# Optimization experiments

Hardware: AMD Instinct MI355X
Metric: run time of the kernel (lower is better)

Reference implementation:

```python
import jax, jax.numpy as jnp
import numpy as np

N_NODES = 50000
N_EDGES = 800000
D_IN = 512
D_OUT = 256

def setup_inputs() -> dict:
    key = jax.random.key(0)
    k1, k2, k3, k4, k5 = jax.random.split(key, 5)
    return {
        "inputs": jax.random.normal(k1, (N_NODES, D_IN), dtype=jnp.float32),
        "weights": jax.random.uniform(k2, (D_IN, D_OUT), dtype=jnp.float32, minval=-0.1, maxval=0.1),
        "bias": jnp.zeros((D_OUT,), dtype=jnp.float32),
        "edge_vals": jax.random.uniform(k3, (N_EDGES,), dtype=jnp.float32),
        "edge_row": jax.random.randint(k4, (N_EDGES,), 0, N_NODES),
        "edge_col": jax.random.randint(k5, (N_EDGES,), 0, N_NODES),
    }

def reference(inputs, weights, bias, edge_vals, edge_row, edge_col):
    # dense projection: [N, D_in] @ [D_in, D_out] -> [N, D_out]
    supports = inputs @ weights
    # sparse adjacency spmm in COO form: out[i] = sum_e vals[e] * supports[col[e]] for row[e] == i
    msgs = supports[edge_col] * edge_vals[:, None]  # [E, D_out]
    aggregated = jax.ops.segment_sum(msgs, edge_row, num_segments=inputs.shape[0])
    return aggregated + bias
```

## Files before the change

### kernel.cpp

```cpp
#include <hip/hip_runtime.h>

#define D_IN 512
#define D_OUT 256
#define BM 128
#define BN 128
#define BK 32

typedef short short8 __attribute__((ext_vector_type(8)));
typedef float floatx4 __attribute__((ext_vector_type(4)));

static __device__ __forceinline__ unsigned short f2bf(float f) {
    unsigned u = __float_as_uint(f);
    u += 0x7FFF + ((u >> 16) & 1);
    return (unsigned short)(u >> 16);
}
static __device__ __forceinline__ float bf2f(unsigned short h) {
    return __uint_as_float((unsigned)h << 16);
}

#define CONV_BLOCKS 256
__global__ __launch_bounds__(512) void convert_and_zero(const float* __restrict__ W,
                                                        unsigned short* __restrict__ Wt,
                                                        int* __restrict__ cnt, int M) {
    int b = blockIdx.x;
    if (b < CONV_BLOCKS) {
        int t = b * 512 + threadIdx.x;
        int n = t >> 9;
        int k = t & 511;
        Wt[t] = f2bf(W[(size_t)k * D_OUT + n]);
    } else {
        int i = (b - CONV_BLOCKS) * 512 + threadIdx.x;
        if (i < M) cnt[i] = 0;
    }
}

__global__ __launch_bounds__(256) void hist_rows(const int* __restrict__ rows,
                                                 int* __restrict__ cnt, int E) {
    int e = blockIdx.x * 256 + threadIdx.x;
    if (e < E) atomicAdd(&cnt[rows[e]], 1);
}

#define SCAN_B 4096
__global__ __launch_bounds__(1024) void scan_blocks(const int* __restrict__ cnt,
                                                    int* __restrict__ ptr,
                                                    int* __restrict__ partials, int M) {
    __shared__ int wsum[16];
    const int t = threadIdx.x, lane = t & 63, wave = t >> 6;
    const int base = blockIdx.x * SCAN_B + t * 4;
    int4 v = make_int4(0, 0, 0, 0);
    if (base + 3 < M) v = *(const int4*)(cnt + base);
    else {
        if (base + 0 < M) v.x = cnt[base + 0];
        if (base + 1 < M) v.y = cnt[base + 1];
        if (base + 2 < M) v.z = cnt[base + 2];
        if (base + 3 < M) v.w = cnt[base + 3];
    }
    int s = v.x + v.y + v.z + v.w;
    int incl = s;
#pragma unroll
    for (int off = 1; off < 64; off <<= 1) {
        int x = __shfl_up(incl, off, 64);
        if (lane >= off) incl += x;
    }
    if (lane == 63) wsum[wave] = incl;
    __syncthreads();
    if (t == 0) {
        int run = 0;
#pragma unroll
        for (int w = 0; w < 16; ++w) { int x = wsum[w]; wsum[w] = run; run += x; }
        partials[blockIdx.x] = run;
    }
    __syncthreads();
    int e0 = wsum[wave] + (incl - s);
    int e1 = e0 + v.x, e2 = e1 + v.y, e3 = e2 + v.z;
    if (base + 3 < M) *(int4*)(ptr + base) = make_int4(e0, e1, e2, e3);
    else {
        if (base + 0 < M) ptr[base + 0] = e0;
        if (base + 1 < M) ptr[base + 1] = e1;
        if (base + 2 < M) ptr[base + 2] = e2;
        if (base + 3 < M) ptr[base + 3] = e3;
    }
}

__global__ __launch_bounds__(256) void add_offsets(int* __restrict__ ptr,
                                                   const int* __restrict__ partials,
                                                   int M) {
    int i = blockIdx.x * 256 + threadIdx.x;
    if (i >= M) return;
    int bucket = blockIdx.x >> 4;
    int off = 0;
    for (int j = 0; j < bucket; ++j) off += partials[j];
    ptr[i] += off;
}

__global__ __launch_bounds__(512, 4) void gemm_build(
    const float* __restrict__ A, const unsigned short* __restrict__ Wt,
    unsigned short* __restrict__ S, int M, int nGemm, int nBuild,
    const float* __restrict__ vals, const int* __restrict__ rows,
    const int* __restrict__ cols, int* __restrict__ ptr,
    unsigned long long* __restrict__ edges, int E) {
    __shared__ unsigned short As[4 * BM * 8];
    __shared__ unsigned short Bs[4 * BN * 8];
    const int bid = blockIdx.x;
    const int tid = threadIdx.x;
    const int r3  = bid % 3;
    const int p3  = bid / 3;

    if (r3 == 2) {
        if (p3 >= nBuild) return;
        int e0 = p3 * 2048 + tid;
        int rr[4]; unsigned cc[4], vv[4]; bool ok[4];
#pragma unroll
        for (int i = 0; i < 4; ++i) {
            int e = e0 + i * 512;
            ok[i] = e < E;
            int es = ok[i] ? e : 0;
            rr[i] = rows[es];
            cc[i] = (unsigned)cols[es];
            vv[i] = (unsigned)__float_as_int(vals[es]);
        }
#pragma unroll
        for (int i = 0; i < 4; ++i) {
            if (ok[i]) {
                int pos = atomicAdd(&ptr[rr[i]], 1);
                unsigned long long packed =
                    (unsigned long long)cc[i] | ((unsigned long long)vv[i] << 32);
                __builtin_nontemporal_store(packed, edges + pos);
            }
        }
        return;
    }

    const int gi = p3 * 2 + r3;
    if (gi >= nGemm) return;
    const int lane = tid & 63;
    const int wave = tid >> 6;
    const int l15  = lane & 15;
    const int quad = lane >> 4;
    const int bm   = (gi >> 1) * BM;
    const int bn   = (gi & 1) * BN;
    const int wm   = (wave >> 2) * 64;
    const int wn   = (wave & 3) * 32;

    const int sm = wave * 16 + l15;
    const bool aval = (bm + sm) < M;
    const float* aptr = A + (size_t)(aval ? bm + sm : 0) * D_IN + quad * 8;
    const unsigned short* bptr = Wt + (size_t)(bn + sm) * D_IN + quad * 8;
    const int soff = (quad * BM + sm) * 8;

    float4 aR0 = aval ? *(const float4*)(aptr + 0) : make_float4(0.f, 0.f, 0.f, 0.f);
    float4 aR1 = aval ? *(const float4*)(aptr + 4) : make_float4(0.f, 0.f, 0.f, 0.f);
    short8 bR  = *(const short8*)bptr;

    floatx4 acc[4][2] = {};

    for (int k0 = 0; k0 < D_IN; k0 += BK) {
        short8 a8;
        a8[0] = (short)f2bf(aR0.x); a8[1] = (short)f2bf(aR0.y);
        a8[2] = (short)f2bf(aR0.z); a8[3] = (short)f2bf(aR0.w);
        a8[4] = (short)f2bf(aR1.x); a8[5] = (short)f2bf(aR1.y);
        a8[6] = (short)f2bf(aR1.z); a8[7] = (short)f2bf(aR1.w);
        *(short8*)(As + soff) = a8;
        *(short8*)(Bs + soff) = bR;
        __syncthreads();

        if (k0 + BK < D_IN) {
            aR0 = aval ? *(const float4*)(aptr + k0 + BK + 0) : make_float4(0.f, 0.f, 0.f, 0.f);
            aR1 = aval ? *(const float4*)(aptr + k0 + BK + 4) : make_float4(0.f, 0.f, 0.f, 0.f);
            bR  = *(const short8*)(bptr + k0 + BK);
        }

        short8 af[4], bfr[2];
#pragma unroll
        for (int i = 0; i < 4; ++i)
            af[i] = *(const short8*)(As + (quad * BM + wm + i * 16 + l15) * 8);
#pragma unroll
        for (int j = 0; j < 2; ++j)
            bfr[j] = *(const short8*)(Bs + (quad * BN + wn + j * 16 + l15) * 8);
#pragma unroll
        for (int i = 0; i < 4; ++i)
#pragma unroll
            for (int j = 0; j < 2; ++j)
                acc[i][j] = __builtin_amdgcn_mfma_f32_16x16x32_bf16(
                    af[i], bfr[j], acc[i][j], 0, 0, 0);
        __syncthreads();
    }

#pragma unroll
    for (int i = 0; i < 4; ++i) {
#pragma unroll
        for (int r = 0; r < 4; ++r) {
            int gm = bm + wm + i * 16 + quad * 4 + r;
            if (gm < M) {
#pragma unroll
                for (int j = 0; j < 2; ++j)
                    S[(size_t)gm * D_OUT + bn + wn + j * 16 + l15] = f2bf(acc[i][j][r]);
            }
        }
    }
}

__global__ __launch_bounds__(256) void spmm_rows(const unsigned short* __restrict__ S,
                                                 const int2* __restrict__ edges,
                                                 const int* __restrict__ ptr,
                                                 const float* __restrict__ bias,
                                                 float* __restrict__ out, int M) {
    const int row = blockIdx.x * 4 + (threadIdx.x >> 6);
    if (row >= M) return;
    const int lane = threadIdx.x & 63;
    float4 a0 = ((const float4*)bias)[lane];
    float4 a1 = make_float4(0.f, 0.f, 0.f, 0.f);
    const int beg = row ? ptr[row - 1] : 0;
    const int end = ptr[row];
    int j = beg;
    for (; j + 7 < end; j += 8) {
        int2 e0 = edges[j + 0], e1 = edges[j + 1], e2 = edges[j + 2], e3 = edges[j + 3];
        int2 e4 = edges[j + 4], e5 = edges[j + 5], e6 = edges[j + 6], e7 = edges[j + 7];
        ushort4 s0 = ((const ushort4*)(S + (size_t)e0.x * D_OUT))[lane];
        ushort4 s1 = ((const ushort4*)(S + (size_t)e1.x * D_OUT))[lane];
        ushort4 s2 = ((const ushort4*)(S + (size_t)e2.x * D_OUT))[lane];
        ushort4 s3 = ((const ushort4*)(S + (size_t)e3.x * D_OUT))[lane];
        ushort4 s4 = ((const ushort4*)(S + (size_t)e4.x * D_OUT))[lane];
        ushort4 s5 = ((const ushort4*)(S + (size_t)e5.x * D_OUT))[lane];
        ushort4 s6 = ((const ushort4*)(S + (size_t)e6.x * D_OUT))[lane];
        ushort4 s7 = ((const ushort4*)(S + (size_t)e7.x * D_OUT))[lane];
        float v0 = __int_as_float(e0.y), v1 = __int_as_float(e1.y);
        float v2 = __int_as_float(e2.y), v3 = __int_as_float(e3.y);
        float v4 = __int_as_float(e4.y), v5 = __int_as_float(e5.y);
        float v6 = __int_as_float(e6.y), v7 = __int_as_float(e7.y);
        a0.x += v0 * bf2f(s0.x) + v2 * bf2f(s2.x) + v4 * bf2f(s4.x) + v6 * bf2f(s6.x);
        a0.y += v0 * bf2f(s0.y) + v2 * bf2f(s2.y) + v4 * bf2f(s4.y) + v6 * bf2f(s6.y);
        a0.z += v0 * bf2f(s0.z) + v2 * bf2f(s2.z) + v4 * bf2f(s4.z) + v6 * bf2f(s6.z);
        a0.w += v0 * bf2f(s0.w) + v2 * bf2f(s2.w) + v4 * bf2f(s4.w) + v6 * bf2f(s6.w);
        a1.x += v1 * bf2f(s1.x) + v3 * bf2f(s3.x) + v5 * bf2f(s5.x) + v7 * bf2f(s7.x);
        a1.y += v1 * bf2f(s1.y) + v3 * bf2f(s3.y) + v5 * bf2f(s5.y) + v7 * bf2f(s7.y);
        a1.z += v1 * bf2f(s1.z) + v3 * bf2f(s3.z) + v5 * bf2f(s5.z) + v7 * bf2f(s7.z);
        a1.w += v1 * bf2f(s1.w) + v3 * bf2f(s3.w) + v5 * bf2f(s5.w) + v7 * bf2f(s7.w);
    }
    for (; j + 3 < end; j += 4) {
        int2 e0 = edges[j], e1 = edges[j + 1], e2 = edges[j + 2], e3 = edges[j + 3];
        ushort4 s0 = ((const ushort4*)(S + (size_t)e0.x * D_OUT))[lane];
        ushort4 s1 = ((const ushort4*)(S + (size_t)e1.x * D_OUT))[lane];
        ushort4 s2 = ((const ushort4*)(S + (size_t)e2.x * D_OUT))[lane];
        ushort4 s3 = ((const ushort4*)(S + (size_t)e3.x * D_OUT))[lane];
        float v0 = __int_as_float(e0.y), v1 = __int_as_float(e1.y);
        float v2 = __int_as_float(e2.y), v3 = __int_as_float(e3.y);
        a0.x += v0 * bf2f(s0.x) + v2 * bf2f(s2.x);
        a0.y += v0 * bf2f(s0.y) + v2 * bf2f(s2.y);
        a0.z += v0 * bf2f(s0.z) + v2 * bf2f(s2.z);
        a0.w += v0 * bf2f(s0.w) + v2 * bf2f(s2.w);
        a1.x += v1 * bf2f(s1.x) + v3 * bf2f(s3.x);
        a1.y += v1 * bf2f(s1.y) + v3 * bf2f(s3.y);
        a1.z += v1 * bf2f(s1.z) + v3 * bf2f(s3.z);
        a1.w += v1 * bf2f(s1.w) + v3 * bf2f(s3.w);
    }
    for (; j < end; ++j) {
        int2 e = edges[j];
        float v = __int_as_float(e.y);
        ushort4 s = ((const ushort4*)(S + (size_t)e.x * D_OUT))[lane];
        a0.x += v * bf2f(s.x);
        a0.y += v * bf2f(s.y);
        a0.z += v * bf2f(s.z);
        a0.w += v * bf2f(s.w);
    }
    a0.x += a1.x; a0.y += a1.y; a0.z += a1.z; a0.w += a1.w;
    floatx4 res = {a0.x, a0.y, a0.z, a0.w};
    __builtin_nontemporal_store(res, (floatx4*)(out + (size_t)row * D_OUT) + lane);
}

extern "C" void kernel_launch(void* const* d_in, const int* in_sizes, int n_in,
                              void* d_out, int out_size, void* d_ws, size_t ws_size,
                              hipStream_t stream) {
    const float* inputs    = (const float*)d_in[0];
    const float* weights   = (const float*)d_in[1];
    const float* bias      = (const float*)d_in[2];
    const float* edge_vals = (const float*)d_in[3];
    const int*   edge_row  = (const int*)d_in[4];
    const int*   edge_col  = (const int*)d_in[5];
    float* out = (float*)d_out;

    const int M = in_sizes[0] / D_IN;
    const int E = in_sizes[3];

    char* ws = (char*)d_ws;
    unsigned short* S  = (unsigned short*)ws;
    unsigned short* Wt = (unsigned short*)(ws + (size_t)M * D_OUT * 2);
    unsigned long long* edges = (unsigned long long*)((char*)Wt + (size_t)D_OUT * D_IN * 2);
    int*  ptr          = (int*)((char*)edges + (size_t)E * 8);
    int*  cnt          = ptr + ((M + 4) & ~3);
    int*  partials     = cnt + M;

    int nzero = (M + 511) / 512;
    convert_and_zero<<<CONV_BLOCKS + nzero, 512, 0, stream>>>(weights, Wt, cnt, M);

    hist_rows<<<(E + 255) / 256, 256, 0, stream>>>(edge_row, cnt, E);
    int nb = (M + SCAN_B - 1) / SCAN_B;
    scan_blocks<<<nb, 1024, 0, stream>>>(cnt, ptr, partials, M);
    add_offsets<<<(M + 255) / 256, 256, 0, stream>>>(ptr, partials, M);

    int nGemm  = 2 * ((M + BM - 1) / BM);
    int nBuild = (E + 2047) / 2048;
    int nPair  = nBuild > (nGemm + 1) / 2 ? nBuild : (nGemm + 1) / 2;
    gemm_build<<<3 * nPair, 512, 0, stream>>>(inputs, Wt, S, M, nGemm, nBuild,
                                              edge_vals, edge_row, edge_col,
                                              ptr, edges, E);

    spmm_rows<<<(M + 3) / 4, 256, 0, stream>>>(S, edges != 0 ? (const int2*)edges : (const int2*)edges, ptr, bias, out, M);
}
```

Before: 332.5 us.

## Retile GEMM to full-width 64x256 blocks and vectorize edge histogram/build

Changes the GEMM tile from 128x128 with BK=32 to 64x256 with BK=64, so each block covers the full output width and reads each A row only once. The fp32 A reads and their bf16 conversion are no longer duplicated across two N-tiles, and there are half as many sync rounds per block. Histogram and edge-build kernels now read rows, cols and vals as int4/float4 vectors with four edges per thread. Build blocks are scheduled first instead of interleaved with GEMM blocks, which may change how the two kinds of work overlap.

New measurement: 333.6 us. No clear change (+0.3%).

```diff
diff --git a/kernel.cpp b/kernel.cpp
--- a/kernel.cpp
+++ b/kernel.cpp
@@ -2,9 +2,9 @@
 
 #define D_IN 512
 #define D_OUT 256
-#define BM 128
-#define BN 128
-#define BK 32
+#define BM 64
+#define BN 256
+#define BK 64
 
 typedef short short8 __attribute__((ext_vector_type(8)));
 typedef float floatx4 __attribute__((ext_vector_type(4)));
@@ -36,8 +36,16 @@
 
 __global__ __launch_bounds__(256) void hist_rows(const int* __restrict__ rows,
                                                  int* __restrict__ cnt, int E) {
-    int e = blockIdx.x * 256 + threadIdx.x;
-    if (e < E) atomicAdd(&cnt[rows[e]], 1);
+    int e0 = (blockIdx.x * 256 + threadIdx.x) * 4;
+    if (e0 + 3 < E) {
+        int4 r = *(const int4*)(rows + e0);
+        atomicAdd(&cnt[r.x], 1);
+        atomicAdd(&cnt[r.y], 1);
+        atomicAdd(&cnt[r.z], 1);
+        atomicAdd(&cnt[r.w], 1);
+    } else {
+        for (int e = e0; e < E; ++e) atomicAdd(&cnt[rows[e]], 1);
+    }
 }
 
 #define SCAN_B 4096
@@ -95,62 +103,72 @@
 
 __global__ __launch_bounds__(512, 4) void gemm_build(
     const float* __restrict__ A, const unsigned short* __restrict__ Wt,
-    unsigned short* __restrict__ S, int M, int nGemm, int nBuild,
+    unsigned short* __restrict__ S, int M, int nBuild,
     const float* __restrict__ vals, const int* __restrict__ rows,
     const int* __restrict__ cols, int* __restrict__ ptr,
     unsigned long long* __restrict__ edges, int E) {
-    __shared__ unsigned short As[4 * BM * 8];
-    __shared__ unsigned short Bs[4 * BN * 8];
+    __shared__ unsigned short As[(BK / 8) * BM * 8];
+    __shared__ unsigned short Bs[(BK / 8) * BN * 8];
     const int bid = blockIdx.x;
     const int tid = threadIdx.x;
-    const int r3  = bid % 3;
-    const int p3  = bid / 3;
-
-    if (r3 == 2) {
-        if (p3 >= nBuild) return;
-        int e0 = p3 * 2048 + tid;
-        int rr[4]; unsigned cc[4], vv[4]; bool ok[4];
-#pragma unroll
-        for (int i = 0; i < 4; ++i) {
-            int e = e0 + i * 512;
-            ok[i] = e < E;
-            int es = ok[i] ? e : 0;
-            rr[i] = rows[es];
-            cc[i] = (unsigned)cols[es];
-            vv[i] = (unsigned)__float_as_int(vals[es]);
-        }
-#pragma unroll
-        for (int i = 0; i < 4; ++i) {
-            if (ok[i]) {
-                int pos = atomicAdd(&ptr[rr[i]], 1);
+
+    if (bid < nBuild) {
+        int e0 = bid * 2048 + tid * 4;
+        if (e0 + 3 < E) {
+            int4   rr = *(const int4*)(rows + e0);
+            int4   cc = *(const int4*)(cols + e0);
+            float4 vv = *(const float4*)(vals + e0);
+            int p0 = atomicAdd(&ptr[rr.x], 1);
+            __builtin_nontemporal_store(
+                (unsigned long long)(unsigned)cc.x |
+                ((unsigned long long)(unsigned)__float_as_int(vv.x) << 32), edges + p0);
+            int p1 = atomicAdd(&ptr[rr.y], 1);
+            __builtin_nontemporal_store(
+                (unsigned long long)(unsigned)cc.y |
+                ((unsigned long long)(unsigned)__float_as_int(vv.y) << 32), edges + p1);
+            int p2 = atomicAdd(&ptr[rr.z], 1);
+            __builtin_nontemporal_store(
+                (unsigned long long)(unsigned)cc.z |
+                ((unsigned long long)(unsigned)__float_as_int(vv.z) << 32), edges + p2);
+            int p3 = atomicAdd(&ptr[rr.w], 1);
+            __builtin_nontemporal_store(
+                (unsigned long long)(unsigned)cc.w |
+                ((unsigned long long)(unsigned)__float_as_int(vv.w) << 32), edges + p3);
+        } else {
+            for (int e = e0; e < E; ++e) {
+                int pos = atomicAdd(&ptr[rows[e]], 1);
                 unsigned long long packed =
-                    (unsigned long long)cc[i] | ((unsigned long long)vv[i] << 32);
+                    (unsigned long long)(unsigned)cols[e] |
+                    ((unsigned long long)(unsigned)__float_as_int(vals[e]) << 32);
                 __builtin_nontemporal_store(packed, edges + pos);
             }
         }
         return;
     }
 
-    const int gi = p3 * 2 + r3;
-    if (gi >= nGemm) return;
+    const int gi   = bid - nBuild;
+    const int bm   = gi * BM;
     const int lane = tid & 63;
     const int wave = tid >> 6;
     const int l15  = lane & 15;
     const int quad = lane >> 4;
-    const int bm   = (gi >> 1) * BM;
-    const int bn   = (gi & 1) * BN;
-    const int wm   = (wave >> 2) * 64;
-    const int wn   = (wave & 3) * 32;
-
-    const int sm = wave * 16 + l15;
-    const bool aval = (bm + sm) < M;
-    const float* aptr = A + (size_t)(aval ? bm + sm : 0) * D_IN + quad * 8;
-    const unsigned short* bptr = Wt + (size_t)(bn + sm) * D_IN + quad * 8;
-    const int soff = (quad * BM + sm) * 8;
+    const int wn   = wave * 32;
+
+    const int ar = (wave & 3) * 16 + l15;
+    const int ap = (wave >> 2) * 4 + quad;
+    const bool aval = (bm + ar) < M;
+    const float* aptr = A + (size_t)(aval ? bm + ar : 0) * D_IN + ap * 8;
+    const int asoff = (ap * BM + ar) * 8;
+
+    const int bn_ = tid >> 1;
+    const int bh  = tid & 1;
+    const unsigned short* bptr = Wt + (size_t)bn_ * D_IN + bh * 32;
 
     float4 aR0 = aval ? *(const float4*)(aptr + 0) : make_float4(0.f, 0.f, 0.f, 0.f);
     float4 aR1 = aval ? *(const float4*)(aptr + 4) : make_float4(0.f, 0.f, 0.f, 0.f);
-    short8 bR  = *(const short8*)bptr;
+    short8 bR[4];
+#pragma unroll
+    for (int j = 0; j < 4; ++j) bR[j] = *(const short8*)(bptr + 8 * j);
 
     floatx4 acc[4][2] = {};
 
@@ -160,29 +178,37 @@
         a8[2] = (short)f2bf(aR0.z); a8[3] = (short)f2bf(aR0.w);
         a8[4] = (short)f2bf(aR1.x); a8[5] = (short)f2bf(aR1.y);
         a8[6] = (short)f2bf(aR1.z); a8[7] = (short)f2bf(aR1.w);
-        *(short8*)(As + soff) = a8;
-        *(short8*)(Bs + soff) = bR;
+        *(short8*)(As + asoff) = a8;
+#pragma unroll
+        for (int j = 0; j < 4; ++j)
+            *(short8*)(Bs + ((bh * 4 + j) * BN + bn_) * 8) = bR[j];
         __syncthreads();
 
         if (k0 + BK < D_IN) {
             aR0 = aval ? *(const float4*)(aptr + k0 + BK + 0) : make_float4(0.f, 0.f, 0.f, 0.f);
             aR1 = aval ? *(const float4*)(aptr + k0 + BK + 4) : make_float4(0.f, 0.f, 0.f, 0.f);
-            bR  = *(const short8*)(bptr + k0 + BK);
+#pragma unroll
+            for (int j = 0; j < 4; ++j)
+                bR[j] = *(const short8*)(bptr + k0 + BK + 8 * j);
         }
 
-        short8 af[4], bfr[2];
-#pragma unroll
-        for (int i = 0; i < 4; ++i)
-            af[i] = *(const short8*)(As + (quad * BM + wm + i * 16 + l15) * 8);
-#pragma unroll
-        for (int j = 0; j < 2; ++j)
-            bfr[j] = *(const short8*)(Bs + (quad * BN + wn + j * 16 + l15) * 8);
-#pragma unroll
-        for (int i = 0; i < 4; ++i)
+#pragma unroll
+        for (int s = 0; s < 2; ++s) {
+            const int p = s * 4 + quad;
+            short8 af[4], bfr[2];
+#pragma unroll
+            for (int i = 0; i < 4; ++i)
+                af[i] = *(const short8*)(As + (p * BM + i * 16 + l15) * 8);
 #pragma unroll
             for (int j = 0; j < 2; ++j)
-                acc[i][j] = __builtin_amdgcn_mfma_f32_16x16x32_bf16(
-                    af[i], bfr[j], acc[i][j], 0, 0, 0);
+                bfr[j] = *(const short8*)(Bs + (p * BN + wn + j * 16 + l15) * 8);
+#pragma unroll
+            for (int i = 0; i < 4; ++i)
+#pragma unroll
+                for (int j = 0; j < 2; ++j)
+                    acc[i][j] = __builtin_amdgcn_mfma_f32_16x16x32_bf16(
+                        af[i], bfr[j], acc[i][j], 0, 0, 0);
+        }
         __syncthreads();
     }
 
@@ -190,11 +216,11 @@
     for (int i = 0; i < 4; ++i) {
 #pragma unroll
         for (int r = 0; r < 4; ++r) {
-            int gm = bm + wm + i * 16 + quad * 4 + r;
+            int gm = bm + i * 16 + quad * 4 + r;
             if (gm < M) {
 #pragma unroll
                 for (int j = 0; j < 2; ++j)
-                    S[(size_t)gm * D_OUT + bn + wn + j * 16 + l15] = f2bf(acc[i][j][r]);
+                    S[(size_t)gm * D_OUT + wn + j * 16 + l15] = f2bf(acc[i][j][r]);
             }
         }
     }
@@ -293,17 +319,16 @@
     int nzero = (M + 511) / 512;
     convert_and_zero<<<CONV_BLOCKS + nzero, 512, 0, stream>>>(weights, Wt, cnt, M);
 
-    hist_rows<<<(E + 255) / 256, 256, 0, stream>>>(edge_row, cnt, E);
+    hist_rows<<<(E + 1023) / 1024, 256, 0, stream>>>(edge_row, cnt, E);
     int nb = (M + SCAN_B - 1) / SCAN_B;
     scan_blocks<<<nb, 1024, 0, stream>>>(cnt, ptr, partials, M);
     add_offsets<<<(M + 255) / 256, 256, 0, stream>>>(ptr, partials, M);
 
-    int nGemm  = 2 * ((M + BM - 1) / BM);
+    int nGemm  = (M + BM - 1) / BM;
     int nBuild = (E + 2047) / 2048;
-    int nPair  = nBuild > (nGemm + 1) / 2 ? nBuild : (nGemm + 1) / 2;
-    gemm_build<<<3 * nPair, 512, 0, stream>>>(inputs, Wt, S, M, nGemm, nBuild,
-                                              edge_vals, edge_row, edge_col,
-                                              ptr, edges, E);
-
-    spmm_rows<<<(M + 3) / 4, 256, 0, stream>>>(S, edges != 0 ? (const int2*)edges : (const int2*)edges, ptr, bias, out, M);
-}
+    gemm_build<<<nBuild + nGemm, 512, 0, stream>>>(inputs, Wt, S, M, nBuild,
+                                                   edge_vals, edge_row, edge_col,
+                                                   ptr, edges, E);
+
+    spmm_rows<<<(M + 3) / 4, 256, 0, stream>>>(S, (const int2*)edges, ptr, bias, out, M);
+}
```
